# Optimization experiments

Hardware: AMD Instinct MI355X
Metric: run time of the kernel (lower is better)

## Reference

```python
import jax, jax.numpy as jnp
import numpy as np

NUM_GRAPHS = 512


def setup_inputs() -> dict:
    key = jax.random.key(0)
    k1, k2, k3, k4, k5 = jax.random.split(key, 5)
    N, D = 131072, 512
    x = jax.random.normal(k1, (N, D), dtype=jnp.float32)
    graph_ptr = jnp.sort(jax.random.randint(k2, (N,), 0, NUM_GRAPHS, dtype=jnp.int64))
    # Linear(dim, dim) params (kaiming-ish scale) and query vector
    W = jax.random.normal(k3, (D, D), dtype=jnp.float32) / np.sqrt(D)
    b = jax.random.normal(k4, (D,), dtype=jnp.float32) * 0.01
    query = jax.random.normal(k5, (D,), dtype=jnp.float32)
    return {"x": x, "graph_ptr": graph_ptr, "W": W, "b": b, "query": query}


def reference(x, graph_ptr, W, b, query):
    # gate: Linear + Tanh, then score = g @ query  -> [N]
    g = jnp.tanh(x @ W.T + b)
    score = g @ query
    seg = graph_ptr.astype(jnp.int32)
    # segmented, numerically-stable softmax over nodes of each graph
    seg_max = jax.ops.segment_max(score, seg, num_segments=NUM_GRAPHS)  # [G]
    # empty segments give -inf max; they have no nodes so gather is safe
    e = jnp.exp(score - seg_max[seg])                                   # [N]
    denom = jax.ops.segment_sum(e, seg, num_segments=NUM_GRAPHS)        # [G]
    attn = e / jnp.where(denom[seg] == 0, 1.0, denom[seg])              # [N]
    # weighted scatter-sum of node features per graph -> [G, D]
    out = jax.ops.segment_sum(attn[:, None] * x, seg, num_segments=NUM_GRAPHS)
    return out
```

## Files before the change

### kernel.cpp

```cpp
#include <hip/hip_runtime.h>

typedef _Float16 f16x8 __attribute__((ext_vector_type(8)));
typedef _Float16 f16x4 __attribute__((ext_vector_type(4)));
typedef __fp16 fp16v2 __attribute__((ext_vector_type(2)));
typedef _Float16 f16v2 __attribute__((ext_vector_type(2)));
typedef short short8 __attribute__((ext_vector_type(8)));
typedef float f32x16 __attribute__((ext_vector_type(16)));

#define DD 512
#define NG 512

typedef __attribute__((address_space(3))) void lds_void;
typedef __attribute__((address_space(1))) void glb_void;

static __device__ __forceinline__ void gload_lds16(const void* g, void* l) {
  __builtin_amdgcn_global_load_lds((const glb_void*)g, (lds_void*)l, 16, 0, 0);
}

#define MEMFENCE asm volatile("" ::: "memory")

static __device__ __forceinline__ f16v2 pk16(float a, float b) {
  fp16v2 p = __builtin_amdgcn_cvt_pkrtz(a, b);
  return __builtin_bit_cast(f16v2, p);
}

static __device__ __forceinline__ float fast_tanh(float v) {
  float e = __expf(2.0f * v);
  return 1.0f - 2.0f * __builtin_amdgcn_rcpf(e + 1.0f);
}

__global__ __launch_bounds__(256) void k_convert_w(const float* __restrict__ W,
                                                   unsigned char* __restrict__ Whl) {
  int t = blockIdx.x * 256 + threadIdx.x;
  int r512 = t >> 6, kg = t & 63;
  int ny = r512 >> 8, col = r512 & 255;
  int ct = col >> 5, c31 = col & 31;
  int kt = kg >> 1, khalf = kg & 1;
  const float* p = W + (size_t)r512 * DD + kg * 8;
  short8 h;
#pragma unroll
  for (int j = 0; j < 8; ++j) {
    _Float16 hh = (_Float16)p[j];
    h[j] = (short)__builtin_bit_cast(unsigned short, hh);
  }
  unsigned char* dst = Whl + (size_t)ny * 262144 + (size_t)kt * 8192 +
                       ct * 1024 + (khalf * 32 + c31) * 16;
  *(short8*)dst = h;
}

__global__ __launch_bounds__(256, 2) void k_gemm_score(
    const float* __restrict__ x, const unsigned char* __restrict__ Whl,
    const float* __restrict__ bias, const float* __restrict__ query,
    float* __restrict__ score_part, int N) {
  __shared__ unsigned char ldsB[3][8192];
  __shared__ unsigned char ldsA[3][4096];
  __shared__ float comb[2][128];
  const int tid = threadIdx.x;
  const int wave = tid >> 6;
  const int lane = tid & 63;
  const int l31 = lane & 31;
  const int kh = lane >> 5;
  const int rg = wave >> 1;
  const int cg = wave & 1;
  const int ny = blockIdx.x;
  const int brow0 = blockIdx.y * 128;

  const unsigned char* wsrc = Whl + (size_t)ny * 262144 +
                              (size_t)wave * 2048 + (size_t)lane * 16;

  const float* asrc = x + (size_t)(brow0 + wave * 32 + (lane >> 2)) * DD + (lane & 3) * 4;
  const int wA = wave * 1024 + (lane >> 2) * 32 + (lane & 3) * 8;
  const int rA0 = (rg * 64 + l31) * 32 + kh * 16;
  const int rA1 = (rg * 64 + 32 + l31) * 32 + kh * 16;

  f32x16 acc[2][4];
#pragma unroll
  for (int f = 0; f < 2; ++f)
#pragma unroll
    for (int j = 0; j < 4; ++j)
#pragma unroll
      for (int r = 0; r < 16; ++r) acc[f][j][r] = 0.f;

#define AISSUE(BUF, KT)                                        \
  do {                                                         \
    const int km_ = (KT) & 31;                                 \
    BUF[0] = *(const float4*)(asrc + km_ * 16);                \
    BUF[1] = *(const float4*)(asrc + km_ * 16 + 16 * DD);      \
  } while (0)

#define BISSUE(KT)                                                        \
  do {                                                                    \
    const int sl_ = (KT) % 3;                                             \
    const unsigned char* sb_ = wsrc + (size_t)((KT) & 31) * 8192;         \
    gload_lds16(sb_, &ldsB[sl_][wave * 2048]);                            \
    gload_lds16(sb_ + 1024, &ldsB[sl_][wave * 2048 + 1024]);              \
  } while (0)

#define AWRITE(BUF, KT)                                                   \
  do {                                                                    \
    const int sl_ = (KT) % 3;                                             \
    f16v2 p0_ = pk16(BUF[0].x, BUF[0].y), p1_ = pk16(BUF[0].z, BUF[0].w); \
    f16v2 p2_ = pk16(BUF[1].x, BUF[1].y), p3_ = pk16(BUF[1].z, BUF[1].w); \
    f16x4 v0_ = {p0_[0], p0_[1], p1_[0], p1_[1]};                         \
    f16x4 v1_ = {p2_[0], p2_[1], p3_[0], p3_[1]};                         \
    *(f16x4*)(&ldsA[sl_][wA]) = v0_;                                      \
    *(f16x4*)(&ldsA[sl_][wA + 512]) = v1_;                  \
  } while (0)

  float4 bufP[2], bufQ[2];
  AISSUE(bufP, 0); MEMFENCE;
  AISSUE(bufQ, 1); MEMFENCE;
  asm volatile("s_waitcnt vmcnt(0)" ::: "memory");
  AWRITE(bufP, 0);
  AWRITE(bufQ, 1);
  MEMFENCE;
  AISSUE(bufP, 2); MEMFENCE;
  BISSUE(0); MEMFENCE;
  AISSUE(bufQ, 3); MEMFENCE;
  BISSUE(1); MEMFENCE;

#define BODY(KT, CUR)                                                     \
  do {                                                                    \
    asm volatile("s_waitcnt vmcnt(4) lgkmcnt(0)" ::: "memory");           \
    __builtin_amdgcn_s_barrier();                                         \
    MEMFENCE;                                                             \
    AWRITE(CUR, (KT) + 2);                                                \
    MEMFENCE;                                                             \
    AISSUE(CUR, (KT) + 4);                                                \
    MEMFENCE;                                                             \
    BISSUE((KT) + 2);                                                     \
    MEMFENCE;                                                             \
    const unsigned char* ab_ = &ldsA[(KT) % 3][0];                        \
    const unsigned char* bb_ = &ldsB[(KT) % 3][lane * 16 + cg * 4096];    \
    f16x8 a0_ = *(const f16x8*)(ab_ + rA0);                               \
    f16x8 a1_ = *(const f16x8*)(ab_ + rA1);                               \
    __builtin_amdgcn_s_setprio(1);                                        \
    _Pragma("unroll")                                                     \
    for (int j = 0; j < 4; ++j) {                                         \
      f16x8 bh_ = *(const f16x8*)(bb_ + j * 1024);                        \
      acc[0][j] = __builtin_amdgcn_mfma_f32_32x32x16_f16(a0_, bh_, acc[0][j], 0, 0, 0); \
      acc[1][j] = __builtin_amdgcn_mfma_f32_32x32x16_f16(a1_, bh_, acc[1][j], 0, 0, 0); \
    }                                                                     \
    __builtin_amdgcn_s_setprio(0);                                        \
  } while (0)

#pragma unroll 1
  for (int it = 0; it < 16; ++it) {
    BODY(it * 2, bufP);
    BODY(it * 2 + 1, bufQ);
  }

  float sp[2][16];
#pragma unroll
  for (int f = 0; f < 2; ++f)
#pragma unroll
    for (int r = 0; r < 16; ++r) sp[f][r] = 0.f;
#pragma unroll
  for (int j = 0; j < 4; ++j) {
    const int col = ny * 256 + (cg * 4 + j) * 32 + l31;
    const float bb2 = bias[col];
    const float qq = query[col];
#pragma unroll
    for (int f = 0; f < 2; ++f)
#pragma unroll
      for (int r = 0; r < 16; ++r)
        sp[f][r] += fast_tanh(acc[f][j][r] + bb2) * qq;
  }
  __syncthreads();
#pragma unroll
  for (int f = 0; f < 2; ++f)
#pragma unroll
    for (int r = 0; r < 16; ++r) {
      float v = sp[f][r];
      v += __shfl_xor(v, 1);
      v += __shfl_xor(v, 2);
      v += __shfl_xor(v, 4);
      v += __shfl_xor(v, 8);
      v += __shfl_xor(v, 16);
      if (l31 == 0)
        comb[cg][rg * 64 + f * 32 + (r & 3) + 8 * (r >> 2) + 4 * kh] = v;
    }
  __syncthreads();
  if (tid < 128)
    score_part[(size_t)ny * N + brow0 + tid] = comb[0][tid] + comb[1][tid];
}

__global__ __launch_bounds__(256) void k_softmax_out(
    const float* __restrict__ x, const void* __restrict__ segp,
    const float* __restrict__ sp0, const float* __restrict__ sp1,
    float* __restrict__ out, int N) {
  const int g = blockIdx.x;
  const int tid = threadIdx.x;

  const long long probe = ((const long long*)segp)[N / 2 - 1];
  const bool is64 = ((unsigned long long)probe < (unsigned long long)NG);
  const long long* s64 = (const long long*)segp;
  const int* s32 = (const int*)segp;

  int s0, s1;
  {
    int lo = 0, hi = N;
    while (lo < hi) {
      int m = (lo + hi) >> 1;
      long long v = is64 ? s64[m] : (long long)s32[m];
      if (v < (long long)g) lo = m + 1; else hi = m;
    }
    s0 = lo;
    lo = s0; hi = N;
    while (lo < hi) {
      int m = (lo + hi) >> 1;
      long long v = is64 ? s64[m] : (long long)s32[m];
      if (v < (long long)(g + 1)) lo = m + 1; else hi = m;
    }
    s1 = lo;
  }

  __shared__ float red[4];
  __shared__ float wbuf[512];

  float lm = -INFINITY;
  for (int i = s0 + tid; i < s1; i += 256) lm = fmaxf(lm, sp0[i] + sp1[i]);
#pragma unroll
  for (int m = 1; m < 64; m <<= 1) lm = fmaxf(lm, __shfl_xor(lm, m));
  if ((tid & 63) == 0) red[tid >> 6] = lm;
  __syncthreads();
  const float mx = fmaxf(fmaxf(red[0], red[1]), fmaxf(red[2], red[3]));
  __syncthreads();

  float ls = 0.f;
  for (int i = s0 + tid; i < s1; i += 256) ls += expf(sp0[i] + sp1[i] - mx);
#pragma unroll
  for (int m = 1; m < 64; m <<= 1) ls += __shfl_xor(ls, m);
  if ((tid & 63) == 0) red[tid >> 6] = ls;
  __syncthreads();
  const float sum = red[0] + red[1] + red[2] + red[3];
  const float inv = sum > 0.f ? 1.0f / sum : 0.f;

  float a0 = 0.f, a1 = 0.f;
  const int c = tid * 2;
  for (int base = s0; base < s1; base += 512) {
    const int cnt = min(512, s1 - base);
    __syncthreads();
    for (int i = tid; i < cnt; i += 256)
      wbuf[i] = expf(sp0[base + i] + sp1[base + i] - mx) * inv;
    __syncthreads();
#pragma unroll 4
    for (int j = 0; j < cnt; ++j) {
      const float w = wbuf[j];
      const float2 xv = *(const float2*)(x + (size_t)(base + j) * DD + c);
      a0 = fmaf(w, xv.x, a0);
      a1 = fmaf(w, xv.y, a1);
    }
  }
  float* op = out + (size_t)g * DD + c;
  op[0] = a0;
  op[1] = a1;
}

extern "C" void kernel_launch(void* const* d_in, const int* in_sizes, int n_in,
                              void* d_out, int out_size, void* d_ws, size_t ws_size,
                              hipStream_t stream) {
  const float* x = (const float*)d_in[0];
  const void* seg = d_in[1];
  const float* W = (const float*)d_in[2];
  const float* b = (const float*)d_in[3];
  const float* q = (const float*)d_in[4];
  float* out = (float*)d_out;
  const int N = in_sizes[0] / DD;

  unsigned char* Whl = (unsigned char*)d_ws;
  float* sp0 = (float*)(Whl + 524288);
  float* sp1 = sp0 + N;

  k_convert_w<<<128, 256, 0, stream>>>(W, Whl);
  dim3 grid(2, N / 128);
  k_gemm_score<<<grid, 256, 0, stream>>>(x, Whl, b, q, sp0, N);
  k_softmax_out<<<NG, 256, 0, stream>>>(x, seg, sp0, sp1, out, N);
}
```

Baseline: 190.5 us.

## Halve GEMM row tile to 64 and raise occupancy to four blocks per CU

```diff
diff --git a/kernel.cpp b/kernel.cpp
--- a/kernel.cpp
+++ b/kernel.cpp
@@ -48,13 +48,13 @@
   *(short8*)dst = h;
 }
 
-__global__ __launch_bounds__(256, 2) void k_gemm_score(
+__global__ __launch_bounds__(256, 4) void k_gemm_score(
     const float* __restrict__ x, const unsigned char* __restrict__ Whl,
     const float* __restrict__ bias, const float* __restrict__ query,
     float* __restrict__ score_part, int N) {
   __shared__ unsigned char ldsB[3][8192];
-  __shared__ unsigned char ldsA[3][4096];
-  __shared__ float comb[2][128];
+  __shared__ unsigned char ldsA[3][2048];
+  __shared__ float comb[2][64];
   const int tid = threadIdx.x;
   const int wave = tid >> 6;
   const int lane = tid & 63;
@@ -63,29 +63,30 @@
   const int rg = wave >> 1;
   const int cg = wave & 1;
   const int ny = blockIdx.x;
-  const int brow0 = blockIdx.y * 128;
+  const int brow0 = blockIdx.y * 64;
 
   const unsigned char* wsrc = Whl + (size_t)ny * 262144 +
                               (size_t)wave * 2048 + (size_t)lane * 16;
 
-  const float* asrc = x + (size_t)(brow0 + wave * 32 + (lane >> 2)) * DD + (lane & 3) * 4;
-  const int wA = wave * 1024 + (lane >> 2) * 32 + (lane & 3) * 8;
-  const int rA0 = (rg * 64 + l31) * 32 + kh * 16;
-  const int rA1 = (rg * 64 + 32 + l31) * 32 + kh * 16;
-
-  f32x16 acc[2][4];
-#pragma unroll
-  for (int f = 0; f < 2; ++f)
-#pragma unroll
-    for (int j = 0; j < 4; ++j)
-#pragma unroll
-      for (int r = 0; r < 16; ++r) acc[f][j][r] = 0.f;
-
-#define AISSUE(BUF, KT)                                        \
-  do {                                                         \
-    const int km_ = (KT) & 31;                                 \
-    BUF[0] = *(const float4*)(asrc + km_ * 16);                \
-    BUF[1] = *(const float4*)(asrc + km_ * 16 + 16 * DD);      \
+  const float* asrc = x + (size_t)(brow0 + (tid >> 2)) * DD + (tid & 3) * 4;
+  const int awoff = ((tid & 3) >> 1) * 1024 + (tid >> 2) * 16 + (tid & 1) * 8;
+  const int aroff = kh * 1024 + (rg * 32 + l31) * 16;
+
+  f32x16 acc[4];
+#pragma unroll
+  for (int j = 0; j < 4; ++j)
+#pragma unroll
+    for (int r = 0; r < 16; ++r) acc[j][r] = 0.f;
+
+#define AISSUE(BUF, KT) do { BUF = *(const float4*)(asrc + ((KT) & 31) * 16); } while (0)
+
+#define AWRITE(BUF, KT)                                                   \
+  do {                                                                    \
+    const int sl_ = (KT) % 3;                                             \
+    f16v2 lo_ = pk16(BUF.x, BUF.y);                                       \
+    f16v2 hi_ = pk16(BUF.z, BUF.w);                                       \
+    f16x4 v_ = {lo_[0], lo_[1], hi_[0], hi_[1]};                          \
+    *(f16x4*)(&ldsA[sl_][awoff]) = v_;                                    \
   } while (0)
 
 #define BISSUE(KT)                                                        \
@@ -96,32 +97,27 @@
     gload_lds16(sb_ + 1024, &ldsB[sl_][wave * 2048 + 1024]);              \
   } while (0)
 
-#define AWRITE(BUF, KT)                                                   \
-  do {                                                                    \
-    const int sl_ = (KT) % 3;                                             \
-    f16v2 p0_ = pk16(BUF[0].x, BUF[0].y), p1_ = pk16(BUF[0].z, BUF[0].w); \
-    f16v2 p2_ = pk16(BUF[1].x, BUF[1].y), p3_ = pk16(BUF[1].z, BUF[1].w); \
-    f16x4 v0_ = {p0_[0], p0_[1], p1_[0], p1_[1]};                         \
-    f16x4 v1_ = {p2_[0], p2_[1], p3_[0], p3_[1]};                         \
-    *(f16x4*)(&ldsA[sl_][wA]) = v0_;                                      \
-    *(f16x4*)(&ldsA[sl_][wA + 512]) = v1_;                  \
-  } while (0)
-
-  float4 bufP[2], bufQ[2];
-  AISSUE(bufP, 0); MEMFENCE;
-  AISSUE(bufQ, 1); MEMFENCE;
+  float4 aP, aQ;
+  AISSUE(aP, 0);
+  MEMFENCE;
+  AISSUE(aQ, 1);
+  MEMFENCE;
   asm volatile("s_waitcnt vmcnt(0)" ::: "memory");
-  AWRITE(bufP, 0);
-  AWRITE(bufQ, 1);
-  MEMFENCE;
-  AISSUE(bufP, 2); MEMFENCE;
-  BISSUE(0); MEMFENCE;
-  AISSUE(bufQ, 3); MEMFENCE;
-  BISSUE(1); MEMFENCE;
+  AWRITE(aP, 0);
+  AWRITE(aQ, 1);
+  MEMFENCE;
+  AISSUE(aP, 2);
+  MEMFENCE;
+  BISSUE(0);
+  MEMFENCE;
+  AISSUE(aQ, 3);
+  MEMFENCE;
+  BISSUE(1);
+  MEMFENCE;
 
 #define BODY(KT, CUR)                                                     \
   do {                                                                    \
-    asm volatile("s_waitcnt vmcnt(4) lgkmcnt(0)" ::: "memory");           \
+    asm volatile("s_waitcnt vmcnt(3) lgkmcnt(0)" ::: "memory");           \
     __builtin_amdgcn_s_barrier();                                         \
     MEMFENCE;                                                             \
     AWRITE(CUR, (KT) + 2);                                                \
@@ -130,58 +126,50 @@
     MEMFENCE;                                                             \
     BISSUE((KT) + 2);                                                     \
     MEMFENCE;                                                             \
-    const unsigned char* ab_ = &ldsA[(KT) % 3][0];                        \
-    const unsigned char* bb_ = &ldsB[(KT) % 3][lane * 16 + cg * 4096];    \
-    f16x8 a0_ = *(const f16x8*)(ab_ + rA0);                               \
-    f16x8 a1_ = *(const f16x8*)(ab_ + rA1);                               \
+    const int slot_ = (KT) % 3;                                           \
+    f16x8 a_ = *(const f16x8*)(&ldsA[slot_][aroff]);                      \
+    const unsigned char* bb_ = &ldsB[slot_][lane * 16 + cg * 4096];       \
     __builtin_amdgcn_s_setprio(1);                                        \
     _Pragma("unroll")                                                     \
     for (int j = 0; j < 4; ++j) {                                         \
       f16x8 bh_ = *(const f16x8*)(bb_ + j * 1024);                        \
-      acc[0][j] = __builtin_amdgcn_mfma_f32_32x32x16_f16(a0_, bh_, acc[0][j], 0, 0, 0); \
-      acc[1][j] = __builtin_amdgcn_mfma_f32_32x32x16_f16(a1_, bh_, acc[1][j], 0, 0, 0); \
+      acc[j] = __builtin_amdgcn_mfma_f32_32x32x16_f16(a_, bh_, acc[j], 0, 0, 0); \
     }                                                                     \
     __builtin_amdgcn_s_setprio(0);                                        \
   } while (0)
 
 #pragma unroll 1
   for (int it = 0; it < 16; ++it) {
-    BODY(it * 2, bufP);
-    BODY(it * 2 + 1, bufQ);
-  }
-
-  float sp[2][16];
-#pragma unroll
-  for (int f = 0; f < 2; ++f)
-#pragma unroll
-    for (int r = 0; r < 16; ++r) sp[f][r] = 0.f;
+    BODY(it * 2, aP);
+    BODY(it * 2 + 1, aQ);
+  }
+
+  float sp[16];
+#pragma unroll
+  for (int r = 0; r < 16; ++r) sp[r] = 0.f;
 #pragma unroll
   for (int j = 0; j < 4; ++j) {
     const int col = ny * 256 + (cg * 4 + j) * 32 + l31;
     const float bb2 = bias[col];
     const float qq = query[col];
 #pragma unroll
-    for (int f = 0; f < 2; ++f)
-#pragma unroll
-      for (int r = 0; r < 16; ++r)
-        sp[f][r] += fast_tanh(acc[f][j][r] + bb2) * qq;
-  }
-  __syncthreads();
-#pragma unroll
-  for (int f = 0; f < 2; ++f)
-#pragma unroll
-    for (int r = 0; r < 16; ++r) {
-      float v = sp[f][r];
-      v += __shfl_xor(v, 1);
-      v += __shfl_xor(v, 2);
-      v += __shfl_xor(v, 4);
-      v += __shfl_xor(v, 8);
-      v += __shfl_xor(v, 16);
-      if (l31 == 0)
-        comb[cg][rg * 64 + f * 32 + (r & 3) + 8 * (r >> 2) + 4 * kh] = v;
-    }
-  __syncthreads();
-  if (tid < 128)
+    for (int r = 0; r < 16; ++r)
+      sp[r] += fast_tanh(acc[j][r] + bb2) * qq;
+  }
+  __syncthreads();
+#pragma unroll
+  for (int r = 0; r < 16; ++r) {
+    float v = sp[r];
+    v += __shfl_xor(v, 1);
+    v += __shfl_xor(v, 2);
+    v += __shfl_xor(v, 4);
+    v += __shfl_xor(v, 8);
+    v += __shfl_xor(v, 16);
+    if (l31 == 0)
+      comb[cg][rg * 32 + (r & 3) + 8 * (r >> 2) + 4 * kh] = v;
+  }
+  __syncthreads();
+  if (tid < 64)
     score_part[(size_t)ny * N + brow0 + tid] = comb[0][tid] + comb[1][tid];
 }
 
@@ -273,7 +261,7 @@
   float* sp1 = sp0 + N;
 
   k_convert_w<<<128, 256, 0, stream>>>(W, Whl);
-  dim3 grid(2, N / 128);
+  dim3 grid(2, N / 64);
   k_gemm_score<<<grid, 256, 0, stream>>>(x, Whl, b, q, sp0, N);
   k_softmax_out<<<NG, 256, 0, stream>>>(x, seg, sp0, sp1, out, N);
 }
```

Result: faster. 180.2 us (-5.4%).
